# Optimization experiments

Measured on AMD Instinct MI355X. Metric: run time of the kernel, lower is better.

Reference implementation:

```python
import jax, jax.numpy as jnp
import numpy as np


def _gru(x, h, Wih, Whh, bih, bhh):
    # torch.nn.GRUCell math. x:(1,in), h:(1,H), Wih:(3H,in), Whh:(3H,H)
    gi = x @ Wih.T + bih
    gh = h @ Whh.T + bhh
    i_r, i_z, i_n = jnp.split(gi, 3, axis=-1)
    h_r, h_z, h_n = jnp.split(gh, 3, axis=-1)
    r = jax.nn.sigmoid(i_r + h_r)
    z = jax.nn.sigmoid(i_z + h_z)
    n = jnp.tanh(i_n + r * h_n)
    return (1.0 - z) * n + z * h


def _combine(S, Wa, ba, va):
    # SelfAttention.combine: additive attention over the stack axis.
    # S:(k,1,H), Wa:(H,A), ba:(A,), va:(A,)
    e = jnp.tanh(S @ Wa + ba) @ va          # (k,1) energies
    w = jax.nn.softmax(e, axis=0)            # softmax over stacked hidden states
    return jnp.sum(w[..., None] * S, axis=0)  # (1,H)


def setup_inputs() -> dict:
    key = jax.random.key(0)
    ks = jax.random.split(key, 20)
    T, F, H, A, L = 16384, 2048, 16, 64, 6
    G = 3 * H
    s = 0.1  # weight scale for numerical sanity
    return {
        "batch": jax.random.normal(ks[0], (T, 1, F), jnp.float32),
        "h0": jax.random.normal(ks[1], (L, 1, H), jnp.float32),
        "W_ih0": jax.random.normal(ks[2], (G, F), jnp.float32) * s,
        "W_hh0": jax.random.normal(ks[3], (G, H), jnp.float32) * s,
        "b_ih0": jax.random.normal(ks[4], (G,), jnp.float32) * s,
        "b_hh0": jax.random.normal(ks[5], (G,), jnp.float32) * s,
        "W_ih": jax.random.normal(ks[6], (L - 1, G, H), jnp.float32) * s,
        "W_hh": jax.random.normal(ks[7], (L - 1, G, H), jnp.float32) * s,
        "b_ih": jax.random.normal(ks[8], (L - 1, G), jnp.float32) * s,
        "b_hh": jax.random.normal(ks[9], (L - 1, G), jnp.float32) * s,
        "Wa": jax.random.normal(ks[10], (L, H, A), jnp.float32) * s,
        "ba": jax.random.normal(ks[11], (L, A), jnp.float32) * s,
        "va": jax.random.normal(ks[12], (L, A), jnp.float32) * s,
        "fc1_w": jax.random.normal(ks[13], (32, H), jnp.float32) * s,
        "fc1_b": jax.random.normal(ks[14], (32,), jnp.float32) * s,
        "fc2_w": jax.random.normal(ks[15], (1, 32), jnp.float32) * s,
        "fc2_b": jax.random.normal(ks[16], (1,), jnp.float32) * s,
    }


def reference(batch, h0, W_ih0, W_hh0, b_ih0, b_hh0, W_ih, W_hh, b_ih, b_hh,
              Wa, ba, va, fc1_w, fc1_b, fc2_w, fc2_b):
    L = Wa.shape[0]

    def step(h_s, x):
        # h_s: (L,1,H) carried hidden states, x: (1,F) current token
        inp = x.reshape(1, -1)
        new = []
        for l in range(L):
            if l == 0:
                inp = _gru(inp, h_s[0], W_ih0, W_hh0, b_ih0, b_hh0)
            else:
                inp = _gru(inp, h_s[l], W_ih[l - 1], W_hh[l - 1], b_ih[l - 1], b_hh[l - 1])
            new.append(inp)
        newS = jnp.stack(new)  # (L,1,H)
        # layer i attends over hidden states of layers i..L-1 (feedback combine)
        h_next = jnp.stack([_combine(newS[i:], Wa[i], ba[i], va[i]) for i in range(L)])
        top = h_next[-1].reshape(-1)  # (H,); dropout is identity in eval mode
        out = (top @ fc1_w.T + fc1_b) @ fc2_w.T + fc2_b  # (1,)
        return h_next, out

    _, outs = jax.lax.scan(step, h0, batch)
    return outs  # (T,1)
```

## Files before the change

kernel.cpp:

```cpp
#include <hip/hip_runtime.h>
#include <cstdint>
#include <cstddef>


#define TT 16384
#define FF 2048
#define HH 16
#define LL 6
#define GG 48
#define CHUNK 64
#define LOG2E 1.44269504088896340736f

__device__ float g_gi0p[(TT + CHUNK) * 64];

__device__ __forceinline__ float exp2_(float x) { return __builtin_amdgcn_exp2f(x); }
__device__ __forceinline__ float rcp_(float x) { return __builtin_amdgcn_rcpf(x); }
__device__ __forceinline__ float sig_n(float s) { return rcp_(1.f + exp2_(s)); }
__device__ __forceinline__ float tanh_p(float s) { return fmaf(-2.f, rcp_(exp2_(s) + 1.f), 1.f); }

#define MEMBAR() __asm__ __volatile__("" ::: "memory")

__device__ __forceinline__ float rdlane(float v, int l) {
  union { float f; int i; } a, b;
  a.f = v; b.i = __builtin_amdgcn_readlane(a.i, l); return b.f;
}
template <int CTRL>
__device__ __forceinline__ float dppf(float v) {
  union { float f; int i; } a, b;
  a.f = v; b.i = __builtin_amdgcn_mov_dpp(a.i, CTRL, 0xF, 0xF, true); return b.f;
}
template <int Q>
__device__ __forceinline__ float qbcast(float v) { return dppf<Q | (Q << 2) | (Q << 4) | (Q << 6)>(v); }

__device__ __forceinline__ float rowsum16(float v) {
  v += dppf<0xB1>(v);
  v += dppf<0x4E>(v);
  v += dppf<0x141>(v);
  v += dppf<0x140>(v);
  return v;
}
__device__ __forceinline__ float dot16r(const float (&w)[16], const float (&h)[16]) {
  float s0 = w[0] * h[0], s1 = w[1] * h[1], s2 = w[2] * h[2], s3 = w[3] * h[3];
#pragma unroll
  for (int k = 4; k < 16; k += 4) {
    s0 = fmaf(w[k], h[k], s0);       s1 = fmaf(w[k + 1], h[k + 1], s1);
    s2 = fmaf(w[k + 2], h[k + 2], s2); s3 = fmaf(w[k + 3], h[k + 3], s3);
  }
  return (s0 + s1) + (s2 + s3);
}
__device__ __forceinline__ float dot16i(const float (&w)[16], const float (&h)[16], float init) {
  float s0 = fmaf(w[0], h[0], init), s1 = w[1] * h[1], s2 = w[2] * h[2], s3 = w[3] * h[3];
#pragma unroll
  for (int k = 4; k < 16; k += 4) {
    s0 = fmaf(w[k], h[k], s0);       s1 = fmaf(w[k + 1], h[k + 1], s1);
    s2 = fmaf(w[k + 2], h[k + 2], s2); s3 = fmaf(w[k + 3], h[k + 3], s3);
  }
  return (s0 + s1) + (s2 + s3);
}

__device__ __forceinline__ int ldAcq(int* f) {
  return __hip_atomic_load(f, __ATOMIC_ACQUIRE, __HIP_MEMORY_SCOPE_WORKGROUP);
}
__device__ __forceinline__ void pollGE(int* f, int target) {
  while (ldAcq(f) < target) {}
}
__device__ __forceinline__ void waitFlag(int* f, int& cache, int need) {
  if (cache < need) { do { cache = ldAcq(f); } while (cache < need); }
}
__device__ __forceinline__ void sigRel(int* f, int v) {
  __hip_atomic_store(f, v, __ATOMIC_RELAXED, __HIP_MEMORY_SCOPE_WORKGROUP);
}

__device__ __forceinline__ void combBlock(const float4 A0, const float4 A1, const float4 A2,
                                          const float4 A3, float nsv,
                                          const float (&Wa)[16], float ba, float va,
                                          const float (&Wh)[16],
                                          float& S, float& ha, float& Pa) {
  float nr[16] = {A0.x, A0.y, A0.z, A0.w, A1.x, A1.y, A1.z, A1.w,
                  A2.x, A2.y, A2.z, A2.w, A3.x, A3.y, A3.z, A3.w};
  float u = dot16i(Wa, nr, ba);
  float P = dot16r(Wh, nr);
  float pe = va * tanh_p(u);
  float r = rowsum16(pe);
  float e = (rdlane(r, 0) + rdlane(r, 16)) + (rdlane(r, 32) + rdlane(r, 48));
  float w = exp2_(e);
  S += w; ha = fmaf(w, nsv, ha); Pa = fmaf(w, P, Pa);
}

__global__ __launch_bounds__(256) void gi0_gemm(const float* __restrict__ X,
                                                const float* __restrict__ W,
                                                const float* __restrict__ bias) {
  __shared__ float xs[64][132];
  __shared__ float ws[48][132];
  const int tid = threadIdx.x;
  const int t0 = blockIdx.x * 64;
  const int tg = tid & 15;
  const int tt = tid >> 4;
  float acc[4][3];
#pragma unroll
  for (int u = 0; u < 4; ++u)
#pragma unroll
    for (int v = 0; v < 3; ++v) acc[u][v] = 0.f;

  for (int k0 = 0; k0 < FF; k0 += 128) {
#pragma unroll
    for (int i = 0; i < 32; ++i) {
      int e = tid + 256 * i; int r = e >> 7, c = e & 127;
      xs[r][c] = X[(size_t)(t0 + r) * FF + k0 + c];
    }
#pragma unroll
    for (int i = 0; i < 24; ++i) {
      int e = tid + 256 * i; int r = e >> 7, c = e & 127;
      ws[r][c] = W[(size_t)r * FF + k0 + c];
    }
    __syncthreads();
#pragma unroll 8
    for (int c = 0; c < 128; ++c) {
      float x0 = xs[tt][c], x1 = xs[tt + 16][c], x2 = xs[tt + 32][c], x3 = xs[tt + 48][c];
      float w0 = ws[tg][c], w1 = ws[tg + 16][c], w2 = ws[tg + 32][c];
      acc[0][0] += x0 * w0; acc[0][1] += x0 * w1; acc[0][2] += x0 * w2;
      acc[1][0] += x1 * w0; acc[1][1] += x1 * w1; acc[1][2] += x1 * w2;
      acc[2][0] += x2 * w0; acc[2][1] += x2 * w1; acc[2][2] += x2 * w2;
      acc[3][0] += x3 * w0; acc[3][1] += x3 * w1; acc[3][2] += x3 * w2;
    }
    __syncthreads();
  }
  const float gsc3[3] = {-LOG2E, -LOG2E, 2.f * LOG2E};
#pragma unroll
  for (int u = 0; u < 4; ++u)
#pragma unroll
    for (int v = 0; v < 3; ++v)
      g_gi0p[(size_t)(t0 + tt + 16 * u) * 64 + tg * 4 + v] =
          (acc[u][v] + bias[tg + 16 * v]) * gsc3[v];
}

__global__ __launch_bounds__(512, 1) void fbrnn_scan(
    const float* __restrict__ h0,
    const float* __restrict__ Whh0, const float* __restrict__ bhh0,
    const float* __restrict__ Wih, const float* __restrict__ Whh,
    const float* __restrict__ bih, const float* __restrict__ bhh,
    const float* __restrict__ Wa, const float* __restrict__ ba,
    const float* __restrict__ va,
    const float* __restrict__ fc1w, const float* __restrict__ fc1b,
    const float* __restrict__ fc2w, const float* __restrict__ fc2b,
    float* __restrict__ out) {
  __shared__ __align__(16) float nsS[2][LL * HH];
  __shared__ __align__(16) float4 recS[5 * 64];
  __shared__ __align__(16) float4 partS[4 * 64];
  __shared__ __align__(16) float nsOut[256 * HH];
  __shared__ __align__(16) float chunkS[2][CHUNK * 64];
  __shared__ int flagNs;
  __shared__ int flagChunk;
  __shared__ int flagOut;
  __shared__ int gen5[2];

  const int tid = threadIdx.x;
  const int wv = tid >> 6;
  const int lane = tid & 63;
  const int qg = lane & 3;
  const int kk = lane >> 2;
  const int gate = (qg < 3 ? qg : 2);
  const int G = gate * 16 + kk;
  const float gsc = (gate == 2) ? 2.f * LOG2E : -LOG2E;

  const bool isChain = (wv == 0);
  const bool isStream = (wv == 4);
  const bool isFc = (wv == 6);
  const int hRow = (wv == 6 || wv == 1) ? 0 : (wv == 2 || wv == 5) ? 1 : -1;
  const int pRow = (wv == 3) ? 2 : (wv == 7) ? 3 : (wv == 5) ? 4 : -1;
  const int pSlot = (wv == 6) ? 0 : (wv == 1) ? 1 : (wv == 2) ? 2 : (wv == 5) ? 3 : -1;

  float WBih[5][16];
  float WB5[16];  float bhh5R = 0.f;
  float Wa0R[16], Wh0R[16], Wa1R[16], Wh1R[16];
  float ba0R = 0.f, va0R = 0.f, bb0 = 0.f;
  float ba1R = 0.f, va1R = 0.f, bb1 = 0.f;
  float WaP[16], WhP[16];
  float baP = 0.f, vaP = 0.f, bhhP = 0.f;
  float WaH[16], WhH[16];
  float baH = 0.f, vaH = 0.f;
  float fc1R[16];
  float fb1 = 0.f, fw2 = 0.f, fb2 = 0.f;

  if (isChain) {
#pragma unroll
    for (int l = 0; l < 5; ++l)
#pragma unroll
      for (int k = 0; k < 16; ++k) WBih[l][k] = Wih[((l * GG) + G) * 16 + k] * gsc;
#pragma unroll
    for (int k = 0; k < 16; ++k) WB5[k] = Whh[(4 * GG + G) * 16 + k] * gsc;
    bhh5R = (bhh[4 * GG + G] + bih[4 * GG + G]) * gsc;
#pragma unroll
    for (int k = 0; k < 16; ++k) {
      Wa0R[k] = Wa[(0 * 16 + k) * 64 + lane] * (2.f * LOG2E);
      Wa1R[k] = Wa[(1 * 16 + k) * 64 + lane] * (2.f * LOG2E);
      Wh0R[k] = Whh0[G * 16 + k] * gsc;
      Wh1R[k] = Whh[(0 * GG + G) * 16 + k] * gsc;
    }
    ba0R = ba[0 * 64 + lane] * (2.f * LOG2E); va0R = va[0 * 64 + lane] * LOG2E;
    ba1R = ba[1 * 64 + lane] * (2.f * LOG2E); va1R = va[1 * 64 + lane] * LOG2E;
    bb0 = bhh0[G] * gsc;
    bb1 = (bhh[0 * GG + G] + bih[0 * GG + G]) * gsc;
  }
  if (pRow >= 0) {
#pragma unroll
    for (int k = 0; k < 16; ++k) WaP[k] = Wa[(pRow * 16 + k) * 64 + lane] * (2.f * LOG2E);
    baP = ba[pRow * 64 + lane] * (2.f * LOG2E);
    vaP = va[pRow * 64 + lane] * LOG2E;
    const float* ws = Whh + ((pRow - 1) * GG + G) * 16;
#pragma unroll
    for (int k = 0; k < 16; ++k) WhP[k] = ws[k] * gsc;
    bhhP = (bhh[(pRow - 1) * GG + G] + bih[(pRow - 1) * GG + G]) * gsc;
  }
  if (hRow >= 0) {
#pragma unroll
    for (int k = 0; k < 16; ++k) WaH[k] = Wa[(hRow * 16 + k) * 64 + lane] * (2.f * LOG2E);
    baH = ba[hRow * 64 + lane] * (2.f * LOG2E);
    vaH = va[hRow * 64 + lane] * LOG2E;
    const float* ws = (hRow == 0) ? (Whh0 + G * 16) : (Whh + ((hRow - 1) * GG + G) * 16);
#pragma unroll
    for (int k = 0; k < 16; ++k) WhH[k] = ws[k] * gsc;
  }
  if (isFc) {
    const int m = lane & 31;
#pragma unroll
    for (int k = 0; k < 16; ++k) fc1R[k] = fc1w[m * 16 + k];
    fb1 = fc1b[m]; fw2 = fc2w[m]; fb2 = fc2b[0];
  }

  if (tid == 0) { flagNs = 0; flagChunk = 1; flagOut = 0; gen5[0] = 0; gen5[1] = 0; }

  float hv5 = 0.f, gh5reg = 0.f;
  float gh0n = 0.f, hv0n = 0.f, gh1n = 0.f, hv1n = 0.f;
  if (isChain) {
    float hr[16];
#pragma unroll
    for (int k = 0; k < 16; ++k) hr[k] = h0[5 * 16 + k];
    hv5 = h0[5 * 16 + kk];
    gh5reg = dot16i(WB5, hr, bhh5R);
#pragma unroll
    for (int k = 0; k < 16; ++k) hr[k] = h0[0 * 16 + k];
    hv0n = h0[0 * 16 + kk];
    gh0n = dot16i(Wh0R, hr, bb0);
#pragma unroll
    for (int k = 0; k < 16; ++k) hr[k] = h0[1 * 16 + k];
    hv1n = h0[1 * 16 + kk];
    gh1n = dot16i(Wh1R, hr, bb1);
  } else if (pRow >= 0) {
    float hr[16];
#pragma unroll
    for (int k = 0; k < 16; ++k) hr[k] = h0[pRow * 16 + k];
    float4 rr;
    rr.x = dot16i(WhP, hr, bhhP);
    rr.y = h0[pRow * 16 + kk];
    rr.z = __int_as_float(0);
    rr.w = 0.f;
    recS[pRow * 64 + lane] = rr;
  }
  if (isStream) {
    const float4* src = (const float4*)g_gi0p;
    float4* dst = (float4*)(&chunkS[0][0]);
#pragma unroll
    for (int q = 0; q < 16; ++q) dst[q * 64 + lane] = src[q * 64 + lane];
  }
  if (pSlot >= 0) partS[pSlot * 64 + lane] = make_float4(0.f, 0.f, 0.f, __int_as_float(0));
  __syncthreads();

#define EBLOCK(J, WaX, baX, vaX, WhX, Sx, hax, Pax) do {                          \
    waitFlag(&flagNs, fcache, t * 8 + (J) + 1);                                   \
    const float4* np_ = (const float4*)&nsS[nb][(J) * 16];                        \
    float4 A0_ = np_[0], A1_ = np_[1], A2_ = np_[2], A3_ = np_[3];                \
    float nsv_ = nsS[nb][(J) * 16 + kk];                                          \
    combBlock(A0_, A1_, A2_, A3_, nsv_, WaX, baX, vaX, WhX, Sx, hax, Pax);        \
  } while (0)

#define TAILFIN(ROW, Sv, hav, Pav) do {                                           \
    float4 A0, A1, A2, A3; float nsv5;                                            \
    for (;;) {                                                                    \
      int g5 = ldAcq(&gen5[nb]);                                                  \
      MEMBAR();                                                                   \
      const float4* np = (const float4*)&nsS[nb][5 * 16];                         \
      A0 = np[0]; A1 = np[1]; A2 = np[2]; A3 = np[3];                             \
      nsv5 = nsS[nb][5 * 16 + kk];                                                \
      MEMBAR();                                                                   \
      if (g5 >= tgt) break;                                                       \
    }                                                                             \
    combBlock(A0, A1, A2, A3, nsv5, WaP, baP, vaP, WhP, Sv, hav, Pav);            \
    const float inv_ = rcp_(Sv);                                                  \
    float4 rr_; rr_.x = fmaf(Pav, inv_, bhhP); rr_.y = hav * inv_;                \
    rr_.z = __int_as_float(tgt); rr_.w = 0.f;                                     \
    recS[(ROW) * 64 + lane] = rr_;                                                \
  } while (0)

  if (isStream) {
#pragma unroll 1
    for (int c = 1; c < 256; ++c) {
      if (c >= 2) pollGE(&flagNs, ((c - 1) * 64 - 1) * 8 + 1);
      const float4* src = (const float4*)(g_gi0p + ((size_t)c << 12));
      float4* dst = (float4*)(&chunkS[c & 1][0]);
#pragma unroll
      for (int q = 0; q < 16; ++q) dst[q * 64 + lane] = src[q * 64 + lane];
      MEMBAR();
      sigRel(&flagChunk, c + 1);
    }
    return;
  }

  if (isFc) {
    int fcache = 0;
#pragma unroll 1
    for (int t = 0; t < TT; ++t) {
      const int nb = t & 1;
      float Sh = 0.f, hah = 0.f, Pah = 0.f;
      EBLOCK(0, WaH, baH, vaH, WhH, Sh, hah, Pah);
      EBLOCK(1, WaH, baH, vaH, WhH, Sh, hah, Pah);
      EBLOCK(2, WaH, baH, vaH, WhH, Sh, hah, Pah);
      partS[0 * 64 + lane] = make_float4(Sh, hah, Pah, __int_as_float(t + 1));
      waitFlag(&flagNs, fcache, t * 8 + 6);
      const float4* np = (const float4*)(nsOut + (t & 255) * 16);
      float4 a0 = np[0], a1 = np[1], a2 = np[2], a3 = np[3];
      float nr[16] = {a0.x, a0.y, a0.z, a0.w, a1.x, a1.y, a1.z, a1.w,
                      a2.x, a2.y, a2.z, a2.w, a3.x, a3.y, a3.z, a3.w};
      float y = dot16i(fc1R, nr, fb1);
      float p = rowsum16(y * fw2);
      float o = rdlane(p, 0) + rdlane(p, 16) + fb2;
      if (lane == 0) out[t] = o;
      MEMBAR();
      sigRel(&flagOut, t + 1);
    }
    return;
  }

  if (!isChain) {
    int fcache = 0;
    if (wv == 1) {
#pragma unroll 1
      for (int t = 0; t < TT; ++t) {
        const int nb = t & 1;
        float Sh = 0.f, hah = 0.f, Pah = 0.f;
        EBLOCK(3, WaH, baH, vaH, WhH, Sh, hah, Pah);
        EBLOCK(4, WaH, baH, vaH, WhH, Sh, hah, Pah);
        partS[1 * 64 + lane] = make_float4(Sh, hah, Pah, __int_as_float(t + 1));
      }
    } else if (wv == 2) {
#pragma unroll 1
      for (int t = 0; t < TT; ++t) {
        const int nb = t & 1;
        float Sh = 0.f, hah = 0.f, Pah = 0.f;
        EBLOCK(1, WaH, baH, vaH, WhH, Sh, hah, Pah);
        EBLOCK(2, WaH, baH, vaH, WhH, Sh, hah, Pah);
        EBLOCK(3, WaH, baH, vaH, WhH, Sh, hah, Pah);
        partS[2 * 64 + lane] = make_float4(Sh, hah, Pah, __int_as_float(t + 1));
      }
    } else if (wv == 5) {
#pragma unroll 1
      for (int t = 0; t < TT; ++t) {
        const int nb = t & 1;
        const int tgt = t + 1;
        float Sh = 0.f, hah = 0.f, Pah = 0.f;
        EBLOCK(4, WaH, baH, vaH, WhH, Sh, hah, Pah);
        partS[3 * 64 + lane] = make_float4(Sh, hah, Pah, __int_as_float(tgt));
        float S = 0.f, ha = 0.f, Pa = 0.f;
        EBLOCK(4, WaP, baP, vaP, WhP, S, ha, Pa);
        TAILFIN(4, S, ha, Pa);
      }
    } else if (wv == 3) {
#pragma unroll 1
      for (int t = 0; t < TT; ++t) {
        const int nb = t & 1;
        const int tgt = t + 1;
        float S = 0.f, ha = 0.f, Pa = 0.f;
        EBLOCK(2, WaP, baP, vaP, WhP, S, ha, Pa);
        EBLOCK(3, WaP, baP, vaP, WhP, S, ha, Pa);
        EBLOCK(4, WaP, baP, vaP, WhP, S, ha, Pa);
        TAILFIN(2, S, ha, Pa);
      }
    } else {
#pragma unroll 1
      for (int t = 0; t < TT; ++t) {
        const int nb = t & 1;
        const int tgt = t + 1;
        float S = 0.f, ha = 0.f, Pa = 0.f;
        EBLOCK(3, WaP, baP, vaP, WhP, S, ha, Pa);
        EBLOCK(4, WaP, baP, vaP, WhP, S, ha, Pa);
        TAILFIN(3, S, ha, Pa);
      }
    }
    return;
  }

  float gnext = chunkS[0][lane];
  float ns_sg[16];
#pragma unroll 1
  for (int t = 0; t < TT; ++t) {
    const int wb = t & 1;

    float ghv[6], hv[6];
    ghv[0] = gh0n; hv[0] = hv0n;
    ghv[1] = gh1n; hv[1] = hv1n;
    ghv[5] = gh5reg; hv[5] = hv5;
    float4 r2, r3, r4;
    float gpre = 0.f;
    float gi0v = gnext;
    float ns = 0.f;
#pragma unroll
    for (int l = 0; l < 6; ++l) {
      if (l == 2) {
        if (!((__float_as_int(r2.z) >= t) & (__float_as_int(r3.z) >= t) &
              (__float_as_int(r4.z) >= t))) {
          do {
            MEMBAR();
            r2 = recS[2 * 64 + lane]; r3 = recS[3 * 64 + lane]; r4 = recS[4 * 64 + lane];
            MEMBAR();
          } while (!((__float_as_int(r2.z) >= t) & (__float_as_int(r3.z) >= t) &
                     (__float_as_int(r4.z) >= t)));
        }
        ghv[2] = r2.x; hv[2] = r2.y;
        ghv[3] = r3.x; hv[3] = r3.y;
        ghv[4] = r4.x; hv[4] = r4.y;
      }
      const float gh_g = ghv[l];
      const float s = (l == 0) ? (gi0v + gh_g) : dot16i(WBih[l - 1], ns_sg, gh_g);
      const float sg = sig_n(s);
      const float smg = s - gh_g;
      const float sr = qbcast<0>(sg);
      const float sz = qbcast<1>(sg);
      const float a = sz * hv[l];
      const float b = 1.f - sz;
      const float tq = tanh_p(fmaf(sr, gh_g, smg));
      ns = fmaf(tq, b, a);
      if (qg == 2) {
        nsS[wb][l * 16 + kk] = ns;
        if (l == 5) nsOut[(t & 255) * 16 + kk] = ns;
      }
      MEMBAR();
      if (l == 5 && lane == 0) { sigRel(&gen5[wb], t + 1); sigRel(&flagNs, t * 8 + 6); }
#pragma unroll
      for (int k = 0; k < 16; ++k) ns_sg[k] = rdlane(ns, 4 * k + 2);
      if (l < 5 && lane == 0) sigRel(&flagNs, t * 8 + l + 1);
      if (l == 0) {
        if ((t & 63) == 63) {
          const int cn = (t + 1) >> 6;
          if (cn < 256) pollGE(&flagChunk, cn + 1);
        }
        if ((t & 63) == 32) pollGE(&flagOut, t - 64);
        gpre = chunkS[((t + 1) >> 6) & 1][((t + 1) & 63) * 64 + lane];
        MEMBAR();
        r2 = recS[2 * 64 + lane]; r3 = recS[3 * 64 + lane]; r4 = recS[4 * 64 + lane];
        MEMBAR();
      }
    }
    const float hv5n = qbcast<2>(ns);
    gh5reg = dot16i(WB5, ns_sg, bhh5R);
    float u0 = dot16i(Wa0R, ns_sg, ba0R);
    float u1 = dot16i(Wa1R, ns_sg, ba1R);
    float P0 = dot16r(Wh0R, ns_sg);
    float P1 = dot16r(Wh1R, ns_sg);
    MEMBAR();
    float4 p0a = partS[0 * 64 + lane], p0b = partS[1 * 64 + lane];
    float4 p1a = partS[2 * 64 + lane], p1b = partS[3 * 64 + lane];
    MEMBAR();
    float pe0 = va0R * tanh_p(u0);
    float pe1 = va1R * tanh_p(u1);
    float rs0 = rowsum16(pe0);
    float rs1 = rowsum16(pe1);
    float e0 = (rdlane(rs0, 0) + rdlane(rs0, 16)) + (rdlane(rs0, 32) + rdlane(rs0, 48));
    float e1 = (rdlane(rs1, 0) + rdlane(rs1, 16)) + (rdlane(rs1, 32) + rdlane(rs1, 48));
    float wj0 = exp2_(e0), wj1 = exp2_(e1);
    const int tp = t + 1;
    if (!((__float_as_int(p0a.w) >= tp) & (__float_as_int(p0b.w) >= tp) &
          (__float_as_int(p1a.w) >= tp) & (__float_as_int(p1b.w) >= tp))) {
      do {
        MEMBAR();
        p0a = partS[0 * 64 + lane]; p0b = partS[1 * 64 + lane];
        p1a = partS[2 * 64 + lane]; p1b = partS[3 * 64 + lane];
        MEMBAR();
      } while (!((__float_as_int(p0a.w) >= tp) & (__float_as_int(p0b.w) >= tp) &
                 (__float_as_int(p1a.w) >= tp) & (__float_as_int(p1b.w) >= tp)));
    }
    float S0 = p0a.x + p0b.x + wj0;
    float hT0 = p0a.y + p0b.y + wj0 * hv5n;
    float PT0 = p0a.z + p0b.z + wj0 * P0;
    float S1 = p1a.x + p1b.x + wj1;
    float hT1 = p1a.y + p1b.y + wj1 * hv5n;
    float PT1 = p1a.z + p1b.z + wj1 * P1;
    const float inv0 = rcp_(S0);
    const float inv1 = rcp_(S1);
    gh0n = fmaf(PT0, inv0, bb0); hv0n = hT0 * inv0;
    gh1n = fmaf(PT1, inv1, bb1); hv1n = hT1 * inv1;
    hv5 = hv5n;
    gnext = gpre;
  }
}

extern "C" void kernel_launch(void* const* d_in, const int* in_sizes, int n_in,
                              void* d_out, int out_size, void* d_ws, size_t ws_size,
                              hipStream_t stream) {
  const float* batch = (const float*)d_in[0];
  const float* h0    = (const float*)d_in[1];
  const float* Wih0  = (const float*)d_in[2];
  const float* Whh0  = (const float*)d_in[3];
  const float* bih0  = (const float*)d_in[4];
  const float* bhh0  = (const float*)d_in[5];
  const float* Wih   = (const float*)d_in[6];
  const float* Whh   = (const float*)d_in[7];
  const float* bih   = (const float*)d_in[8];
  const float* bhh   = (const float*)d_in[9];
  const float* Wa    = (const float*)d_in[10];
  const float* ba    = (const float*)d_in[11];
  const float* va    = (const float*)d_in[12];
  const float* fc1w  = (const float*)d_in[13];
  const float* fc1b  = (const float*)d_in[14];
  const float* fc2w  = (const float*)d_in[15];
  const float* fc2b  = (const float*)d_in[16];
  float* out = (float*)d_out;
  (void)in_sizes; (void)n_in; (void)out_size; (void)d_ws; (void)ws_size;

  gi0_gemm<<<TT / 64, 256, 0, stream>>>(batch, Wih0, bih0);
  fbrnn_scan<<<1, 512, 0, stream>>>(h0, Whh0, bhh0, Wih, Whh, bih, bhh,
                                    Wa, ba, va, fc1w, fc1b, fc2w, fc2b, out);
}
```

Before: 22.11 ms.

## Rebalance attention-combine work across waves with per-row sequence flags

Replaces the single global flagNs counter with per-row sequence words stored next to each hidden-state row. Consumers spin on the row data itself instead of a shared flag. The combine work is redistributed across seven helper waves with 12 partial-sum slots, so the chain wave and tail rows gather more, smaller partials. The chunk-streaming wave is merged into the FC wave, which prefetches the next gi0 chunk into registers. The GRU update is also refactored to carry h-1, saving an op on the critical chain. The cost is more partial-sum polling and reads per step, plus higher register use in the FC wave.

```diff
diff --git a/kernel.cpp b/kernel.cpp
--- a/kernel.cpp
+++ b/kernel.cpp
@@ -9,6 +9,7 @@
 #define LL 6
 #define GG 48
 #define CHUNK 64
+#define NSR 20
 #define LOG2E 1.44269504088896340736f
 
 __device__ float g_gi0p[(TT + CHUNK) * 64];
@@ -61,11 +62,11 @@
 __device__ __forceinline__ int ldAcq(int* f) {
   return __hip_atomic_load(f, __ATOMIC_ACQUIRE, __HIP_MEMORY_SCOPE_WORKGROUP);
 }
+__device__ __forceinline__ int ldRlx(int* f) {
+  return __hip_atomic_load(f, __ATOMIC_RELAXED, __HIP_MEMORY_SCOPE_WORKGROUP);
+}
 __device__ __forceinline__ void pollGE(int* f, int target) {
   while (ldAcq(f) < target) {}
-}
-__device__ __forceinline__ void waitFlag(int* f, int& cache, int need) {
-  if (cache < need) { do { cache = ldAcq(f); } while (cache < need); }
 }
 __device__ __forceinline__ void sigRel(int* f, int v) {
   __hip_atomic_store(f, v, __ATOMIC_RELAXED, __HIP_MEMORY_SCOPE_WORKGROUP);
@@ -144,15 +145,13 @@
     const float* __restrict__ fc1w, const float* __restrict__ fc1b,
     const float* __restrict__ fc2w, const float* __restrict__ fc2b,
     float* __restrict__ out) {
-  __shared__ __align__(16) float nsS[2][LL * HH];
+  __shared__ __align__(16) float nsS[2 * LL * NSR];
+  __shared__ __align__(16) float nsOut[256 * NSR];
   __shared__ __align__(16) float4 recS[5 * 64];
-  __shared__ __align__(16) float4 partS[4 * 64];
-  __shared__ __align__(16) float nsOut[256 * HH];
+  __shared__ __align__(16) float4 partS[12 * 64];
   __shared__ __align__(16) float chunkS[2][CHUNK * 64];
-  __shared__ int flagNs;
   __shared__ int flagChunk;
   __shared__ int flagOut;
-  __shared__ int gen5[2];
 
   const int tid = threadIdx.x;
   const int wv = tid >> 6;
@@ -164,23 +163,33 @@
   const float gsc = (gate == 2) ? 2.f * LOG2E : -LOG2E;
 
   const bool isChain = (wv == 0);
-  const bool isStream = (wv == 4);
-  const bool isFc = (wv == 6);
-  const int hRow = (wv == 6 || wv == 1) ? 0 : (wv == 2 || wv == 5) ? 1 : -1;
-  const int pRow = (wv == 3) ? 2 : (wv == 7) ? 3 : (wv == 5) ? 4 : -1;
-  const int pSlot = (wv == 6) ? 0 : (wv == 1) ? 1 : (wv == 2) ? 2 : (wv == 5) ? 3 : -1;
+  const bool isW4 = (wv == 4);
 
   float WBih[5][16];
   float WB5[16];  float bhh5R = 0.f;
   float Wa0R[16], Wh0R[16], Wa1R[16], Wh1R[16];
   float ba0R = 0.f, va0R = 0.f, bb0 = 0.f;
   float ba1R = 0.f, va1R = 0.f, bb1 = 0.f;
-  float WaP[16], WhP[16];
-  float baP = 0.f, vaP = 0.f, bhhP = 0.f;
-  float WaH[16], WhH[16];
-  float baH = 0.f, vaH = 0.f;
-  float fc1R[16];
-  float fb1 = 0.f, fw2 = 0.f, fb2 = 0.f;
+  float WaA[16], WhA[16]; float baA = 0.f, vaA = 0.f;
+  float WaB[16], WhB[16]; float baB = 0.f, vaB = 0.f;
+  float WaC[16], WhC[16]; float baC = 0.f, vaC = 0.f;
+  float WaT[16], WhT[16]; float baT = 0.f, vaT = 0.f, bhT = 0.f;
+  float fc1R[16]; float fb1 = 0.f, fw2 = 0.f, fb2 = 0.f;
+
+#define LOADROW(R, WaX, baX, vaX, WhX) do {                                      \
+    _Pragma("unroll") for (int k = 0; k < 16; ++k)                               \
+      WaX[k] = Wa[((R) * 16 + k) * 64 + lane] * (2.f * LOG2E);                   \
+    baX = ba[(R) * 64 + lane] * (2.f * LOG2E);                                   \
+    vaX = va[(R) * 64 + lane] * LOG2E;                                           \
+    { const float* ws_ = ((R) == 0) ? (Whh0 + G * 16)                            \
+                                    : (Whh + (((R) - 1) * GG + G) * 16);         \
+      _Pragma("unroll") for (int k = 0; k < 16; ++k) WhX[k] = ws_[k] * gsc; }    \
+  } while (0)
+#define LOADBH(R, bhX) do {                                                      \
+    bhX = (((R) == 0) ? bhh0[G]                                                  \
+                      : (bhh[((R) - 1) * GG + G] + bih[((R) - 1) * GG + G])) *   \
+          gsc;                                                                   \
+  } while (0)
 
   if (isChain) {
 #pragma unroll
@@ -190,135 +199,127 @@
 #pragma unroll
     for (int k = 0; k < 16; ++k) WB5[k] = Whh[(4 * GG + G) * 16 + k] * gsc;
     bhh5R = (bhh[4 * GG + G] + bih[4 * GG + G]) * gsc;
-#pragma unroll
-    for (int k = 0; k < 16; ++k) {
-      Wa0R[k] = Wa[(0 * 16 + k) * 64 + lane] * (2.f * LOG2E);
-      Wa1R[k] = Wa[(1 * 16 + k) * 64 + lane] * (2.f * LOG2E);
-      Wh0R[k] = Whh0[G * 16 + k] * gsc;
-      Wh1R[k] = Whh[(0 * GG + G) * 16 + k] * gsc;
-    }
-    ba0R = ba[0 * 64 + lane] * (2.f * LOG2E); va0R = va[0 * 64 + lane] * LOG2E;
-    ba1R = ba[1 * 64 + lane] * (2.f * LOG2E); va1R = va[1 * 64 + lane] * LOG2E;
-    bb0 = bhh0[G] * gsc;
-    bb1 = (bhh[0 * GG + G] + bih[0 * GG + G]) * gsc;
-  }
-  if (pRow >= 0) {
-#pragma unroll
-    for (int k = 0; k < 16; ++k) WaP[k] = Wa[(pRow * 16 + k) * 64 + lane] * (2.f * LOG2E);
-    baP = ba[pRow * 64 + lane] * (2.f * LOG2E);
-    vaP = va[pRow * 64 + lane] * LOG2E;
-    const float* ws = Whh + ((pRow - 1) * GG + G) * 16;
-#pragma unroll
-    for (int k = 0; k < 16; ++k) WhP[k] = ws[k] * gsc;
-    bhhP = (bhh[(pRow - 1) * GG + G] + bih[(pRow - 1) * GG + G]) * gsc;
-  }
-  if (hRow >= 0) {
-#pragma unroll
-    for (int k = 0; k < 16; ++k) WaH[k] = Wa[(hRow * 16 + k) * 64 + lane] * (2.f * LOG2E);
-    baH = ba[hRow * 64 + lane] * (2.f * LOG2E);
-    vaH = va[hRow * 64 + lane] * LOG2E;
-    const float* ws = (hRow == 0) ? (Whh0 + G * 16) : (Whh + ((hRow - 1) * GG + G) * 16);
-#pragma unroll
-    for (int k = 0; k < 16; ++k) WhH[k] = ws[k] * gsc;
-  }
-  if (isFc) {
+    LOADROW(0, Wa0R, ba0R, va0R, Wh0R); LOADBH(0, bb0);
+    LOADROW(1, Wa1R, ba1R, va1R, Wh1R); LOADBH(1, bb1);
+  } else if (isW4) {
     const int m = lane & 31;
 #pragma unroll
     for (int k = 0; k < 16; ++k) fc1R[k] = fc1w[m * 16 + k];
     fb1 = fc1b[m]; fw2 = fc2w[m]; fb2 = fc2b[0];
-  }
-
-  if (tid == 0) { flagNs = 0; flagChunk = 1; flagOut = 0; gen5[0] = 0; gen5[1] = 0; }
-
-  float hv5 = 0.f, gh5reg = 0.f;
-  float gh0n = 0.f, hv0n = 0.f, gh1n = 0.f, hv1n = 0.f;
+  } else if (wv == 1) {
+    LOADROW(0, WaA, baA, vaA, WhA);
+    LOADROW(2, WaB, baB, vaB, WhB);
+  } else if (wv == 2) {
+    LOADROW(0, WaA, baA, vaA, WhA);
+    LOADROW(3, WaT, baT, vaT, WhT); LOADBH(3, bhT);
+  } else if (wv == 3) {
+    LOADROW(1, WaA, baA, vaA, WhA);
+    LOADROW(4, WaT, baT, vaT, WhT); LOADBH(4, bhT);
+  } else if (wv == 5) {
+    LOADROW(0, WaA, baA, vaA, WhA);
+    LOADROW(1, WaB, baB, vaB, WhB);
+    LOADROW(2, WaT, baT, vaT, WhT); LOADBH(2, bhT);
+  } else if (wv == 6) {
+    LOADROW(1, WaA, baA, vaA, WhA);
+    LOADROW(2, WaB, baB, vaB, WhB);
+    LOADROW(3, WaC, baC, vaC, WhC);
+  } else {
+    LOADROW(2, WaA, baA, vaA, WhA);
+    LOADROW(3, WaB, baB, vaB, WhB);
+    LOADROW(4, WaC, baC, vaC, WhC);
+  }
+
+  if (tid == 0) { flagChunk = 1; flagOut = 0; }
+  for (int i = tid; i < 2 * LL; i += 512) ((int*)nsS)[i * NSR + 16] = 0;
+  for (int i = tid; i < 256; i += 512) ((int*)nsOut)[i * NSR + 16] = 0;
+  if (wv == 6) {
+#pragma unroll
+    for (int s = 0; s < 12; ++s)
+      partS[s * 64 + lane] = make_float4(0.f, 0.f, 0.f, __int_as_float(0));
+  }
+
+  float hv0m = 0.f, gh0n = 0.f, hv1m = 0.f, gh1n = 0.f;
+  float hv5m = 0.f, gh5reg = 0.f;
   if (isChain) {
     float hr[16];
 #pragma unroll
     for (int k = 0; k < 16; ++k) hr[k] = h0[5 * 16 + k];
-    hv5 = h0[5 * 16 + kk];
+    hv5m = h0[5 * 16 + kk] - 1.f;
     gh5reg = dot16i(WB5, hr, bhh5R);
 #pragma unroll
     for (int k = 0; k < 16; ++k) hr[k] = h0[0 * 16 + k];
-    hv0n = h0[0 * 16 + kk];
+    hv0m = h0[0 * 16 + kk] - 1.f;
     gh0n = dot16i(Wh0R, hr, bb0);
 #pragma unroll
     for (int k = 0; k < 16; ++k) hr[k] = h0[1 * 16 + k];
-    hv1n = h0[1 * 16 + kk];
+    hv1m = h0[1 * 16 + kk] - 1.f;
     gh1n = dot16i(Wh1R, hr, bb1);
-  } else if (pRow >= 0) {
+  }
+  const int tailRow = (wv == 5) ? 2 : (wv == 2) ? 3 : (wv == 3) ? 4 : -1;
+  if (tailRow >= 0) {
     float hr[16];
 #pragma unroll
-    for (int k = 0; k < 16; ++k) hr[k] = h0[pRow * 16 + k];
+    for (int k = 0; k < 16; ++k) hr[k] = h0[tailRow * 16 + k];
     float4 rr;
-    rr.x = dot16i(WhP, hr, bhhP);
-    rr.y = h0[pRow * 16 + kk];
-    rr.z = __int_as_float(0);
-    rr.w = 0.f;
-    recS[pRow * 64 + lane] = rr;
-  }
-  if (isStream) {
+    rr.x = dot16i(WhT, hr, bhT);
+    rr.y = h0[tailRow * 16 + kk] - 1.f;
+    rr.z = __int_as_float(0); rr.w = 0.f;
+    recS[tailRow * 64 + lane] = rr;
+  }
+
+  float4 pf0, pf1, pf2, pf3, pf4, pf5, pf6, pf7;
+  float4 pf8, pf9, pfA, pfB, pfC, pfD, pfE, pfF;
+  if (isW4) {
     const float4* src = (const float4*)g_gi0p;
     float4* dst = (float4*)(&chunkS[0][0]);
 #pragma unroll
     for (int q = 0; q < 16; ++q) dst[q * 64 + lane] = src[q * 64 + lane];
-  }
-  if (pSlot >= 0) partS[pSlot * 64 + lane] = make_float4(0.f, 0.f, 0.f, __int_as_float(0));
+    const float4* s1 = (const float4*)(g_gi0p + ((size_t)1 << 12));
+    pf0 = s1[0 * 64 + lane]; pf1 = s1[1 * 64 + lane]; pf2 = s1[2 * 64 + lane];
+    pf3 = s1[3 * 64 + lane]; pf4 = s1[4 * 64 + lane]; pf5 = s1[5 * 64 + lane];
+    pf6 = s1[6 * 64 + lane]; pf7 = s1[7 * 64 + lane]; pf8 = s1[8 * 64 + lane];
+    pf9 = s1[9 * 64 + lane]; pfA = s1[10 * 64 + lane]; pfB = s1[11 * 64 + lane];
+    pfC = s1[12 * 64 + lane]; pfD = s1[13 * 64 + lane]; pfE = s1[14 * 64 + lane];
+    pfF = s1[15 * 64 + lane];
+  }
   __syncthreads();
 
-#define EBLOCK(J, WaX, baX, vaX, WhX, Sx, hax, Pax) do {                          \
-    waitFlag(&flagNs, fcache, t * 8 + (J) + 1);                                   \
-    const float4* np_ = (const float4*)&nsS[nb][(J) * 16];                        \
-    float4 A0_ = np_[0], A1_ = np_[1], A2_ = np_[2], A3_ = np_[3];                \
-    float nsv_ = nsS[nb][(J) * 16 + kk];                                          \
+#define SBLOCK(J, WaX, baX, vaX, WhX, Sx, hax, Pax) do {                          \
+    float* base_ = &nsS[(nb * LL + (J)) * NSR];                                   \
+    float4 A0_, A1_, A2_, A3_; float nsv_;                                        \
+    for (;;) {                                                                    \
+      int st_ = ldRlx((int*)(base_ + 16));                                        \
+      MEMBAR();                                                                   \
+      A0_ = ((const float4*)base_)[0]; A1_ = ((const float4*)base_)[1];           \
+      A2_ = ((const float4*)base_)[2]; A3_ = ((const float4*)base_)[3];           \
+      nsv_ = base_[kk];                                                           \
+      MEMBAR();                                                                   \
+      if (st_ >= tgt) break;                                                      \
+    }                                                                             \
     combBlock(A0_, A1_, A2_, A3_, nsv_, WaX, baX, vaX, WhX, Sx, hax, Pax);        \
   } while (0)
 
-#define TAILFIN(ROW, Sv, hav, Pav) do {                                           \
-    float4 A0, A1, A2, A3; float nsv5;                                            \
-    for (;;) {                                                                    \
-      int g5 = ldAcq(&gen5[nb]);                                                  \
-      MEMBAR();                                                                   \
-      const float4* np = (const float4*)&nsS[nb][5 * 16];                         \
-      A0 = np[0]; A1 = np[1]; A2 = np[2]; A3 = np[3];                             \
-      nsv5 = nsS[nb][5 * 16 + kk];                                                \
-      MEMBAR();                                                                   \
-      if (g5 >= tgt) break;                                                       \
-    }                                                                             \
-    combBlock(A0, A1, A2, A3, nsv5, WaP, baP, vaP, WhP, Sv, hav, Pav);            \
-    const float inv_ = rcp_(Sv);                                                  \
-    float4 rr_; rr_.x = fmaf(Pav, inv_, bhhP); rr_.y = hav * inv_;                \
-    rr_.z = __int_as_float(tgt); rr_.w = 0.f;                                     \
-    recS[(ROW) * 64 + lane] = rr_;                                                \
+#define POSTP(SLOT, Sx, hax, Pax) do {                                            \
+    MEMBAR();                                                                     \
+    partS[(SLOT) * 64 + lane] = make_float4(Sx, hax, Pax, __int_as_float(tgt));   \
+    MEMBAR();                                                                     \
   } while (0)
 
-  if (isStream) {
-#pragma unroll 1
-    for (int c = 1; c < 256; ++c) {
-      if (c >= 2) pollGE(&flagNs, ((c - 1) * 64 - 1) * 8 + 1);
-      const float4* src = (const float4*)(g_gi0p + ((size_t)c << 12));
-      float4* dst = (float4*)(&chunkS[c & 1][0]);
-#pragma unroll
-      for (int q = 0; q < 16; ++q) dst[q * 64 + lane] = src[q * 64 + lane];
-      MEMBAR();
-      sigRel(&flagChunk, c + 1);
-    }
-    return;
-  }
-
-  if (isFc) {
-    int fcache = 0;
+  if (isW4) {
+    int cNext = 1;
 #pragma unroll 1
     for (int t = 0; t < TT; ++t) {
-      const int nb = t & 1;
-      float Sh = 0.f, hah = 0.f, Pah = 0.f;
-      EBLOCK(0, WaH, baH, vaH, WhH, Sh, hah, Pah);
-      EBLOCK(1, WaH, baH, vaH, WhH, Sh, hah, Pah);
-      EBLOCK(2, WaH, baH, vaH, WhH, Sh, hah, Pah);
-      partS[0 * 64 + lane] = make_float4(Sh, hah, Pah, __int_as_float(t + 1));
-      waitFlag(&flagNs, fcache, t * 8 + 6);
-      const float4* np = (const float4*)(nsOut + (t & 255) * 16);
-      float4 a0 = np[0], a1 = np[1], a2 = np[2], a3 = np[3];
+      const int tgt = t + 1;
+      float* nb_ = nsOut + (t & 255) * NSR;
+      float4 a0, a1, a2, a3;
+      for (;;) {
+        int st = ldRlx((int*)(nb_ + 16));
+        MEMBAR();
+        a0 = ((const float4*)nb_)[0]; a1 = ((const float4*)nb_)[1];
+        a2 = ((const float4*)nb_)[2]; a3 = ((const float4*)nb_)[3];
+        MEMBAR();
+        if (st >= tgt) break;
+      }
       float nr[16] = {a0.x, a0.y, a0.z, a0.w, a1.x, a1.y, a1.z, a1.w,
                       a2.x, a2.y, a2.z, a2.w, a3.x, a3.y, a3.z, a3.w};
       float y = dot16i(fc1R, nr, fb1);
@@ -326,64 +327,154 @@
       float o = rdlane(p, 0) + rdlane(p, 16) + fb2;
       if (lane == 0) out[t] = o;
       MEMBAR();
-      sigRel(&flagOut, t + 1);
+      sigRel(&flagOut, tgt);
+      if ((t & 63) == 48 && cNext < 256) {
+        float4* dst = (float4*)(&chunkS[cNext & 1][0]);
+        dst[0 * 64 + lane] = pf0;  dst[1 * 64 + lane] = pf1;
+        dst[2 * 64 + lane] = pf2;  dst[3 * 64 + lane] = pf3;
+        dst[4 * 64 + lane] = pf4;  dst[5 * 64 + lane] = pf5;
+        dst[6 * 64 + lane] = pf6;  dst[7 * 64 + lane] = pf7;
+        dst[8 * 64 + lane] = pf8;  dst[9 * 64 + lane] = pf9;
+        dst[10 * 64 + lane] = pfA; dst[11 * 64 + lane] = pfB;
+        dst[12 * 64 + lane] = pfC; dst[13 * 64 + lane] = pfD;
+        dst[14 * 64 + lane] = pfE; dst[15 * 64 + lane] = pfF;
+        MEMBAR();
+        sigRel(&flagChunk, cNext + 1);
+        ++cNext;
+        if (cNext < 256) {
+          const float4* s1 = (const float4*)(g_gi0p + ((size_t)cNext << 12));
+          pf0 = s1[0 * 64 + lane]; pf1 = s1[1 * 64 + lane]; pf2 = s1[2 * 64 + lane];
+          pf3 = s1[3 * 64 + lane]; pf4 = s1[4 * 64 + lane]; pf5 = s1[5 * 64 + lane];
+          pf6 = s1[6 * 64 + lane]; pf7 = s1[7 * 64 + lane]; pf8 = s1[8 * 64 + lane];
+          pf9 = s1[9 * 64 + lane]; pfA = s1[10 * 64 + lane]; pfB = s1[11 * 64 + lane];
+          pfC = s1[12 * 64 + lane]; pfD = s1[13 * 64 + lane]; pfE = s1[14 * 64 + lane];
+          pfF = s1[15 * 64 + lane];
+        }
+      }
     }
     return;
   }
 
   if (!isChain) {
-    int fcache = 0;
     if (wv == 1) {
 #pragma unroll 1
       for (int t = 0; t < TT; ++t) {
-        const int nb = t & 1;
-        float Sh = 0.f, hah = 0.f, Pah = 0.f;
-        EBLOCK(3, WaH, baH, vaH, WhH, Sh, hah, Pah);
-        EBLOCK(4, WaH, baH, vaH, WhH, Sh, hah, Pah);
-        partS[1 * 64 + lane] = make_float4(Sh, hah, Pah, __int_as_float(t + 1));
+        const int nb = t & 1; const int tgt = t + 1;
+        float S = 0.f, ha = 0.f, Pa = 0.f;
+        SBLOCK(0, WaA, baA, vaA, WhA, S, ha, Pa);
+        SBLOCK(3, WaA, baA, vaA, WhA, S, ha, Pa);
+        POSTP(0, S, ha, Pa);
+        S = 0.f; ha = 0.f; Pa = 0.f;
+        SBLOCK(4, WaB, baB, vaB, WhB, S, ha, Pa);
+        POSTP(8, S, ha, Pa);
       }
     } else if (wv == 2) {
 #pragma unroll 1
       for (int t = 0; t < TT; ++t) {
-        const int nb = t & 1;
-        float Sh = 0.f, hah = 0.f, Pah = 0.f;
-        EBLOCK(1, WaH, baH, vaH, WhH, Sh, hah, Pah);
-        EBLOCK(2, WaH, baH, vaH, WhH, Sh, hah, Pah);
-        EBLOCK(3, WaH, baH, vaH, WhH, Sh, hah, Pah);
-        partS[2 * 64 + lane] = make_float4(Sh, hah, Pah, __int_as_float(t + 1));
+        const int nb = t & 1; const int tgt = t + 1;
+        float S = 0.f, ha = 0.f, Pa = 0.f;
+        SBLOCK(1, WaA, baA, vaA, WhA, S, ha, Pa);
+        SBLOCK(4, WaA, baA, vaA, WhA, S, ha, Pa);
+        POSTP(1, S, ha, Pa);
+        S = 0.f; ha = 0.f; Pa = 0.f;
+        SBLOCK(5, WaT, baT, vaT, WhT, S, ha, Pa);
+        float4 m0, m1;
+        for (;;) {
+          MEMBAR();
+          m0 = partS[9 * 64 + lane]; m1 = partS[10 * 64 + lane];
+          MEMBAR();
+          int ok = (__float_as_int(m0.w) >= tgt) & (__float_as_int(m1.w) >= tgt);
+          if (__all(ok)) break;
+        }
+        S += m0.x + m1.x; ha += m0.y + m1.y; Pa += m0.z + m1.z;
+        const float inv = rcp_(S);
+        float4 rr; rr.x = fmaf(Pa, inv, bhT); rr.y = fmaf(ha, inv, -1.f);
+        rr.z = __int_as_float(tgt); rr.w = 0.f;
+        MEMBAR();
+        recS[3 * 64 + lane] = rr;
+        MEMBAR();
+      }
+    } else if (wv == 3) {
+#pragma unroll 1
+      for (int t = 0; t < TT; ++t) {
+        const int nb = t & 1; const int tgt = t + 1;
+        float S = 0.f, ha = 0.f, Pa = 0.f;
+        SBLOCK(1, WaA, baA, vaA, WhA, S, ha, Pa);
+        SBLOCK(4, WaA, baA, vaA, WhA, S, ha, Pa);
+        POSTP(3, S, ha, Pa);
+        S = 0.f; ha = 0.f; Pa = 0.f;
+        SBLOCK(5, WaT, baT, vaT, WhT, S, ha, Pa);
+        float4 m0;
+        for (;;) {
+          MEMBAR();
+          m0 = partS[11 * 64 + lane];
+          MEMBAR();
+          if (__all(__float_as_int(m0.w) >= tgt)) break;
+        }
+        S += m0.x; ha += m0.y; Pa += m0.z;
+        const float inv = rcp_(S);
+        float4 rr; rr.x = fmaf(Pa, inv, bhT); rr.y = fmaf(ha, inv, -1.f);
+        rr.z = __int_as_float(tgt); rr.w = 0.f;
+        MEMBAR();
+        recS[4 * 64 + lane] = rr;
+        MEMBAR();
       }
     } else if (wv == 5) {
 #pragma unroll 1
       for (int t = 0; t < TT; ++t) {
-        const int nb = t & 1;
-        const int tgt = t + 1;
-        float Sh = 0.f, hah = 0.f, Pah = 0.f;
-        EBLOCK(4, WaH, baH, vaH, WhH, Sh, hah, Pah);
-        partS[3 * 64 + lane] = make_float4(Sh, hah, Pah, __int_as_float(tgt));
+        const int nb = t & 1; const int tgt = t + 1;
         float S = 0.f, ha = 0.f, Pa = 0.f;
-        EBLOCK(4, WaP, baP, vaP, WhP, S, ha, Pa);
-        TAILFIN(4, S, ha, Pa);
-      }
-    } else if (wv == 3) {
+        SBLOCK(2, WaA, baA, vaA, WhA, S, ha, Pa);
+        POSTP(2, S, ha, Pa);
+        S = 0.f; ha = 0.f; Pa = 0.f;
+        SBLOCK(3, WaB, baB, vaB, WhB, S, ha, Pa);
+        POSTP(5, S, ha, Pa);
+        S = 0.f; ha = 0.f; Pa = 0.f;
+        SBLOCK(5, WaT, baT, vaT, WhT, S, ha, Pa);
+        float4 m0, m1, m2;
+        for (;;) {
+          MEMBAR();
+          m0 = partS[6 * 64 + lane]; m1 = partS[7 * 64 + lane]; m2 = partS[8 * 64 + lane];
+          MEMBAR();
+          int ok = (__float_as_int(m0.w) >= tgt) & (__float_as_int(m1.w) >= tgt) &
+                   (__float_as_int(m2.w) >= tgt);
+          if (__all(ok)) break;
+        }
+        S += m0.x + m1.x + m2.x; ha += m0.y + m1.y + m2.y; Pa += m0.z + m1.z + m2.z;
+        const float inv = rcp_(S);
+        float4 rr; rr.x = fmaf(Pa, inv, bhT); rr.y = fmaf(ha, inv, -1.f);
+        rr.z = __int_as_float(tgt); rr.w = 0.f;
+        MEMBAR();
+        recS[2 * 64 + lane] = rr;
+        MEMBAR();
+      }
+    } else if (wv == 6) {
 #pragma unroll 1
       for (int t = 0; t < TT; ++t) {
-        const int nb = t & 1;
-        const int tgt = t + 1;
+        const int nb = t & 1; const int tgt = t + 1;
         float S = 0.f, ha = 0.f, Pa = 0.f;
-        EBLOCK(2, WaP, baP, vaP, WhP, S, ha, Pa);
-        EBLOCK(3, WaP, baP, vaP, WhP, S, ha, Pa);
-        EBLOCK(4, WaP, baP, vaP, WhP, S, ha, Pa);
-        TAILFIN(2, S, ha, Pa);
+        SBLOCK(2, WaA, baA, vaA, WhA, S, ha, Pa);
+        POSTP(4, S, ha, Pa);
+        S = 0.f; ha = 0.f; Pa = 0.f;
+        SBLOCK(3, WaB, baB, vaB, WhB, S, ha, Pa);
+        POSTP(7, S, ha, Pa);
+        S = 0.f; ha = 0.f; Pa = 0.f;
+        SBLOCK(4, WaC, baC, vaC, WhC, S, ha, Pa);
+        POSTP(10, S, ha, Pa);
       }
     } else {
 #pragma unroll 1
       for (int t = 0; t < TT; ++t) {
-        const int nb = t & 1;
-        const int tgt = t + 1;
+        const int nb = t & 1; const int tgt = t + 1;
         float S = 0.f, ha = 0.f, Pa = 0.f;
-        EBLOCK(3, WaP, baP, vaP, WhP, S, ha, Pa);
-        EBLOCK(4, WaP, baP, vaP, WhP, S, ha, Pa);
-        TAILFIN(3, S, ha, Pa);
+        SBLOCK(2, WaA, baA, vaA, WhA, S, ha, Pa);
+        POSTP(6, S, ha, Pa);
+        S = 0.f; ha = 0.f; Pa = 0.f;
+        SBLOCK(3, WaB, baB, vaB, WhB, S, ha, Pa);
+        POSTP(9, S, ha, Pa);
+        S = 0.f; ha = 0.f; Pa = 0.f;
+        SBLOCK(4, WaC, baC, vaC, WhC, S, ha, Pa);
+        POSTP(11, S, ha, Pa);
       }
     }
     return;
@@ -395,10 +486,10 @@
   for (int t = 0; t < TT; ++t) {
     const int wb = t & 1;
 
-    float ghv[6], hv[6];
-    ghv[0] = gh0n; hv[0] = hv0n;
-    ghv[1] = gh1n; hv[1] = hv1n;
-    ghv[5] = gh5reg; hv[5] = hv5;
+    float ghv[6], hvm1[6];
+    ghv[0] = gh0n; hvm1[0] = hv0m;
+    ghv[1] = gh1n; hvm1[1] = hv1m;
+    ghv[5] = gh5reg; hvm1[5] = hv5m;
     float4 r2, r3, r4;
     float gpre = 0.f;
     float gi0v = gnext;
@@ -415,9 +506,9 @@
           } while (!((__float_as_int(r2.z) >= t) & (__float_as_int(r3.z) >= t) &
                      (__float_as_int(r4.z) >= t)));
         }
-        ghv[2] = r2.x; hv[2] = r2.y;
-        ghv[3] = r3.x; hv[3] = r3.y;
-        ghv[4] = r4.x; hv[4] = r4.y;
+        ghv[2] = r2.x; hvm1[2] = r2.y;
+        ghv[3] = r3.x; hvm1[3] = r3.y;
+        ghv[4] = r4.x; hvm1[4] = r4.y;
       }
       const float gh_g = ghv[l];
       const float s = (l == 0) ? (gi0v + gh_g) : dot16i(WBih[l - 1], ns_sg, gh_g);
@@ -425,19 +516,23 @@
       const float smg = s - gh_g;
       const float sr = qbcast<0>(sg);
       const float sz = qbcast<1>(sg);
-      const float a = sz * hv[l];
-      const float b = 1.f - sz;
-      const float tq = tanh_p(fmaf(sr, gh_g, smg));
-      ns = fmaf(tq, b, a);
+      const float nb2 = fmaf(2.f, sz, -2.f);
+      const float apb = fmaf(sz, hvm1[l], 1.f);
+      const float E = exp2_(fmaf(sr, gh_g, smg));
+      const float R = rcp_(E + 1.f);
+      ns = fmaf(nb2, R, apb);
       if (qg == 2) {
-        nsS[wb][l * 16 + kk] = ns;
-        if (l == 5) nsOut[(t & 255) * 16 + kk] = ns;
+        nsS[(wb * LL + l) * NSR + kk] = ns;
+        if (l == 5) nsOut[(t & 255) * NSR + kk] = ns;
       }
       MEMBAR();
-      if (l == 5 && lane == 0) { sigRel(&gen5[wb], t + 1); sigRel(&flagNs, t * 8 + 6); }
+      if (qg == 2 && kk == 0) {
+        sigRel((int*)&nsS[(wb * LL + l) * NSR + 16], t + 1);
+        if (l == 5) sigRel((int*)&nsOut[(t & 255) * NSR + 16], t + 1);
+      }
+      MEMBAR();
 #pragma unroll
       for (int k = 0; k < 16; ++k) ns_sg[k] = rdlane(ns, 4 * k + 2);
-      if (l < 5 && lane == 0) sigRel(&flagNs, t * 8 + l + 1);
       if (l == 0) {
         if ((t & 63) == 63) {
           const int cn = (t + 1) >> 6;
@@ -450,16 +545,16 @@
         MEMBAR();
       }
     }
+    MEMBAR();
+    float4 q0 = partS[0 * 64 + lane], q1 = partS[1 * 64 + lane], q2 = partS[2 * 64 + lane];
+    float4 q3 = partS[3 * 64 + lane], q4 = partS[4 * 64 + lane], q5 = partS[5 * 64 + lane];
+    MEMBAR();
     const float hv5n = qbcast<2>(ns);
     gh5reg = dot16i(WB5, ns_sg, bhh5R);
     float u0 = dot16i(Wa0R, ns_sg, ba0R);
     float u1 = dot16i(Wa1R, ns_sg, ba1R);
     float P0 = dot16r(Wh0R, ns_sg);
     float P1 = dot16r(Wh1R, ns_sg);
-    MEMBAR();
-    float4 p0a = partS[0 * 64 + lane], p0b = partS[1 * 64 + lane];
-    float4 p1a = partS[2 * 64 + lane], p1b = partS[3 * 64 + lane];
-    MEMBAR();
     float pe0 = va0R * tanh_p(u0);
     float pe1 = va1R * tanh_p(u1);
     float rs0 = rowsum16(pe0);
@@ -468,27 +563,29 @@
     float e1 = (rdlane(rs1, 0) + rdlane(rs1, 16)) + (rdlane(rs1, 32) + rdlane(rs1, 48));
     float wj0 = exp2_(e0), wj1 = exp2_(e1);
     const int tp = t + 1;
-    if (!((__float_as_int(p0a.w) >= tp) & (__float_as_int(p0b.w) >= tp) &
-          (__float_as_int(p1a.w) >= tp) & (__float_as_int(p1b.w) >= tp))) {
+    if (!((__float_as_int(q0.w) >= tp) & (__float_as_int(q1.w) >= tp) &
+          (__float_as_int(q2.w) >= tp) & (__float_as_int(q3.w) >= tp) &
+          (__float_as_int(q4.w) >= tp) & (__float_as_int(q5.w) >= tp))) {
       do {
         MEMBAR();
-        p0a = partS[0 * 64 + lane]; p0b = partS[1 * 64 + lane];
-        p1a = partS[2 * 64 + lane]; p1b = partS[3 * 64 + lane];
-        MEMBAR();
-      } while (!((__float_as_int(p0a.w) >= tp) & (__float_as_int(p0b.w) >= tp) &
-                 (__float_as_int(p1a.w) >= tp) & (__float_as_int(p1b.w) >= tp)));
+        q0 = partS[0 * 64 + lane]; q1 = partS[1 * 64 + lane]; q2 = partS[2 * 64 + lane];
+        q3 = partS[3 * 64 + lane]; q4 = partS[4 * 64 + lane]; q5 = partS[5 * 64 + lane];
+        MEMBAR();
+      } while (!((__float_as_int(q0.w) >= tp) & (__float_as_int(q1.w) >= tp) &
+                 (__float_as_int(q2.w) >= tp) & (__float_as_int(q3.w) >= tp) &
+                 (__float_as_int(q4.w) >= tp) & (__float_as_int(q5.w) >= tp)));
     }
-    float S0 = p0a.x + p0b.x + wj0;
-    float hT0 = p0a.y + p0b.y + wj0 * hv5n;
-    float PT0 = p0a.z + p0b.z + wj0 * P0;
-    float S1 = p1a.x + p1b.x + wj1;
-    float hT1 = p1a.y + p1b.y + wj1 * hv5n;
-    float PT1 = p1a.z + p1b.z + wj1 * P1;
+    float S0 = q0.x + q1.x + q2.x + wj0;
+    float hT0 = q0.y + q1.y + q2.y + wj0 * hv5n;
+    float PT0 = q0.z + q1.z + q2.z + wj0 * P0;
+    float S1 = q3.x + q4.x + q5.x + wj1;
+    float hT1 = q3.y + q4.y + q5.y + wj1 * hv5n;
+    float PT1 = q3.z + q4.z + q5.z + wj1 * P1;
     const float inv0 = rcp_(S0);
     const float inv1 = rcp_(S1);
-    gh0n = fmaf(PT0, inv0, bb0); hv0n = hT0 * inv0;
-    gh1n = fmaf(PT1, inv1, bb1); hv1n = hT1 * inv1;
-    hv5 = hv5n;
+    gh0n = fmaf(PT0, inv0, bb0); hv0m = fmaf(hT0, inv0, -1.f);
+    gh1n = fmaf(PT1, inv1, bb1); hv1m = fmaf(hT1, inv1, -1.f);
+    hv5m = hv5n - 1.f;
     gnext = gpre;
   }
 }
```

Result: slower. 66.05 ms (+198.8%).
